# Kernel tuning notes

Hardware: AMD Instinct MI355X
Metric: run time of the kernel (lower is better)

The kernel has to match this reference:

```python
import jax, jax.numpy as jnp
import numpy as np

N, E = 50000, 600000
D_IN, D_H, D_OUT, D_E = 128, 128, 128, 32


def setup_inputs() -> dict:
    key = jax.random.key(0)
    ks = jax.random.split(key, 20)
    s = 0.05
    inp = {
        "x": jax.random.normal(ks[0], (N, D_IN), dtype=jnp.float32),
        "edge_index": jax.random.randint(ks[1], (2, E), 0, N, dtype=jnp.int64),
        "edge_attr": jax.random.normal(ks[2], (E, D_E), dtype=jnp.float32),
        # layer 0 (GINEConv MLP + edge lin: edge_dim -> in_channels)
        "w1_0": jax.random.normal(ks[3], (D_IN, D_H), dtype=jnp.float32) * s,
        "b1_0": jnp.zeros((D_H,), jnp.float32),
        "w2_0": jax.random.normal(ks[4], (D_H, D_H), dtype=jnp.float32) * s,
        "b2_0": jnp.zeros((D_H,), jnp.float32),
        "we_0": jax.random.normal(ks[5], (D_E, D_IN), dtype=jnp.float32) * s,
        "be_0": jnp.zeros((D_IN,), jnp.float32),
        # layer 1 (edge lin: edge_dim -> hidden_channels)
        "w1_1": jax.random.normal(ks[6], (D_H, D_H), dtype=jnp.float32) * s,
        "b1_1": jnp.zeros((D_H,), jnp.float32),
        "w2_1": jax.random.normal(ks[7], (D_H, D_H), dtype=jnp.float32) * s,
        "b2_1": jnp.zeros((D_H,), jnp.float32),
        "we_1": jax.random.normal(ks[8], (D_E, D_H), dtype=jnp.float32) * s,
        "be_1": jnp.zeros((D_H,), jnp.float32),
        # output head
        "fc1_w": jax.random.normal(ks[9], (D_H, D_H), dtype=jnp.float32) * s,
        "fc1_b": jnp.zeros((D_H,), jnp.float32),
        "fc2_w": jax.random.normal(ks[10], (D_H, D_OUT), dtype=jnp.float32) * s,
        "fc2_b": jnp.zeros((D_OUT,), jnp.float32),
    }
    return inp


def _gine_layer(x, src, dst, edge_attr, we, be, w1, b1, w2, b2):
    # GINEConv (eps=0): out = MLP(x + sum_j ReLU(x_j + edge_lin(e_ij)))
    e_emb = edge_attr @ we + be                       # [E, d]
    msg = jax.nn.relu(x[src] + e_emb)                 # gather + message
    agg = jax.ops.segment_sum(msg, dst, num_segments=x.shape[0])  # scatter-add
    h = agg + x                                       # (1 + eps) * x, eps = 0
    return jnp.maximum(h @ w1 + b1, 0.0) @ w2 + b2    # 2-layer MLP


def reference(x, edge_index, edge_attr,
              w1_0, b1_0, w2_0, b2_0, we_0, be_0,
              w1_1, b1_1, w2_1, b2_1, we_1, be_1,
              fc1_w, fc1_b, fc2_w, fc2_b):
    src, dst = edge_index[0], edge_index[1]
    h = _gine_layer(x, src, dst, edge_attr, we_0, be_0, w1_0, b1_0, w2_0, b2_0)
    h = jax.nn.relu(h)  # activation (dropout=0 -> identity)
    h = _gine_layer(h, src, dst, edge_attr, we_1, be_1, w1_1, b1_1, w2_1, b2_1)
    h = jax.nn.relu(h)
    h = jax.nn.relu(h @ fc1_w + fc1_b)
    return h @ fc2_w + fc2_b
```

## Files before the change

### kernel.cpp

```cpp
#include <hip/hip_runtime.h>
#include <stdint.h>


#define ND 128
#define ED 32

typedef __attribute__((ext_vector_type(8))) short short8;
typedef __attribute__((ext_vector_type(4))) float f32x4;

__device__ inline unsigned short bf16_hi(float f) {
    union { float f; unsigned u; } v;
    v.f = f;
    return (unsigned short)(v.u >> 16);
}
__device__ inline float bf16_f(unsigned short h) {
    union { unsigned u; float f; } v;
    v.u = ((unsigned)h) << 16;
    return v.f;
}

__global__ __launch_bounds__(256) void zero_kernel(int* __restrict__ p, int n) {
    int i = blockIdx.x * blockDim.x + threadIdx.x;
    if (i < n) p[i] = 0;
}

__global__ __launch_bounds__(256) void hist_kernel(const int* __restrict__ ei,
                                                   int* __restrict__ counts, int E) {
    int i = blockIdx.x * blockDim.x + threadIdx.x;
    if (i < E) atomicAdd(&counts[ei[E + i]], 1);
}

__global__ __launch_bounds__(256) void bsum_kernel(const int* __restrict__ counts,
                                                   int* __restrict__ bsum, int N) {
    __shared__ int s[256];
    int t = threadIdx.x;
    int i = blockIdx.x * 256 + t;
    s[t] = (i < N) ? counts[i] : 0;
    __syncthreads();
#pragma unroll
    for (int off = 128; off > 0; off >>= 1) {
        if (t < off) s[t] += s[t + off];
        __syncthreads();
    }
    if (t == 0) bsum[blockIdx.x] = s[0];
}

__global__ __launch_bounds__(256) void scan_bsums(const int* __restrict__ bsum,
                                                  int* __restrict__ bofs,
                                                  int* __restrict__ row_start_N, int NB) {
    __shared__ int s[256];
    int t = threadIdx.x;
    int chunk = (NB + 255) >> 8;
    int lo = min(t * chunk, NB);
    int hi = min(lo + chunk, NB);
    int sum = 0;
    for (int i = lo; i < hi; ++i) sum += bsum[i];
    s[t] = sum;
    __syncthreads();
    for (int off = 1; off < 256; off <<= 1) {
        int v = (t >= off) ? s[t - off] : 0;
        __syncthreads();
        s[t] += v;
        __syncthreads();
    }
    int pre = (t == 0) ? 0 : s[t - 1];
    for (int i = lo; i < hi; ++i) {
        bofs[i] = pre;
        pre += bsum[i];
    }
    if (t == 255) *row_start_N = s[255];
}

__global__ __launch_bounds__(256) void expand_kernel(const int* __restrict__ counts,
                                                     const int* __restrict__ bofs,
                                                     int* __restrict__ row_start,
                                                     int* __restrict__ woff, int N) {
    __shared__ int s[256];
    int t = threadIdx.x;
    int i = blockIdx.x * 256 + t;
    int c = (i < N) ? counts[i] : 0;
    s[t] = c;
    __syncthreads();
    for (int off = 1; off < 256; off <<= 1) {
        int v = (t >= off) ? s[t - off] : 0;
        __syncthreads();
        s[t] += v;
        __syncthreads();
    }
    if (i < N) {
        int pre = bofs[blockIdx.x] + s[t] - c;
        row_start[i] = pre;
        woff[i] = pre;
    }
}

__global__ __launch_bounds__(256) void scatter_kernel(const int* __restrict__ ei,
                                                      int* __restrict__ woff,
                                                      int4* __restrict__ pack, int E) {
    int i = blockIdx.x * blockDim.x + threadIdx.x;
    if (i < E) {
        int d = ei[E + i];
        int p = atomicAdd(&woff[d], 1);
        pack[p] = make_int4(ei[i], i, d, 0);
    }
}

__global__ __launch_bounds__(256) void wprep_kernel(
    const float* __restrict__ w0, const float* __restrict__ w1,
    const float* __restrict__ w2, const float* __restrict__ w3,
    const float* __restrict__ w4, const float* __restrict__ w5,
    unsigned short* __restrict__ hi, unsigned short* __restrict__ lo) {
    int t = blockIdx.x * blockDim.x + threadIdx.x;
    const float* W;
    switch (blockIdx.y) {
        case 0: W = w0; break;
        case 1: W = w1; break;
        case 2: W = w2; break;
        case 3: W = w3; break;
        case 4: W = w4; break;
        default: W = w5; break;
    }
    unsigned short* dh = hi + (size_t)blockIdx.y * 16384;
    unsigned short* dl = lo + (size_t)blockIdx.y * 16384;
    int c = t >> 6, l = t & 63;
    int nt = c >> 2, ks = c & 3;
    int n = nt * 16 + (l & 15);
    int kb = ks * 32 + ((l >> 4) << 3);
#pragma unroll
    for (int j = 0; j < 8; ++j) {
        float f = W[(size_t)(kb + j) * ND + n];
        unsigned short h = bf16_hi(f);
        dh[((size_t)c * 64 + l) * 8 + j] = h;
        dl[((size_t)c * 64 + l) * 8 + j] = bf16_hi(f - bf16_f(h));
    }
}

__global__ __launch_bounds__(256) void wprep_we(const float* __restrict__ w0,
                                                const float* __restrict__ w1,
                                                unsigned short* __restrict__ hi) {
    int t = threadIdx.x;
    int c = (blockIdx.x << 2) + (t >> 6);
    int l = t & 63;
    const float* W = blockIdx.y ? w1 : w0;
    unsigned short* dh = hi + (size_t)blockIdx.y * 4096;
    int n = c * 16 + (l & 15);
    int kb = (l >> 4) << 3;
#pragma unroll
    for (int j = 0; j < 8; ++j)
        dh[((size_t)c * 64 + l) * 8 + j] = bf16_hi(W[(size_t)(kb + j) * ND + n]);
}

__global__ __launch_bounds__(256, 4) void agg_mfma(
    const float* __restrict__ xin, const float* __restrict__ edge_attr,
    const unsigned short* __restrict__ bfh, const float* __restrict__ be,
    const int* __restrict__ row_start, const int4* __restrict__ pack,
    float* __restrict__ hout, int N, int NW) {
    int lane = threadIdx.x & 63;
    int gw = (blockIdx.x * blockDim.x + threadIdx.x) >> 6;
    int m = lane & 15;
    int quad = lane >> 4;

    short8 bh[8];
#pragma unroll
    for (int nt = 0; nt < 8; ++nt)
        bh[nt] = *(const short8*)(bfh + ((size_t)nt * 64 + lane) * 8);
    float ber[8];
#pragma unroll
    for (int nt = 0; nt < 8; ++nt) ber[nt] = be[nt * 16 + m];

    for (int v = gw; v < N; v += NW) {
        int beg = row_start[v];
        int end = row_start[v + 1];
        float part[8];
#pragma unroll
        for (int nt = 0; nt < 8; ++nt) part[nt] = 0.f;

        for (int base = beg; base < end; base += 16) {
            int rem = end - base;
            int mm = m < rem ? m : rem - 1;
            int4 pk = pack[base + mm];
            int s[4];
#pragma unroll
            for (int r = 0; r < 4; ++r) s[r] = __shfl(pk.x, quad * 4 + r, 64);

            const float4* ar = (const float4*)(edge_attr + (size_t)pk.y * ED + quad * 8);
            float4 a0 = ar[0], a1 = ar[1];
            float xv[4][8];
#pragma unroll
            for (int r = 0; r < 4; ++r) {
                const float* xr = xin + (size_t)s[r] * ND + m;
#pragma unroll
                for (int nt = 0; nt < 8; ++nt) xv[r][nt] = xr[nt * 16];
            }

            float af[8] = {a0.x, a0.y, a0.z, a0.w, a1.x, a1.y, a1.z, a1.w};
            short8 ah, al;
#pragma unroll
            for (int j = 0; j < 8; ++j) {
                unsigned short h = bf16_hi(af[j]);
                ah[j] = (short)h;
                al[j] = (short)bf16_hi(af[j] - bf16_f(h));
            }

#pragma unroll
            for (int nt = 0; nt < 8; ++nt) {
                f32x4 a = {0.f, 0.f, 0.f, 0.f};
                a = __builtin_amdgcn_mfma_f32_16x16x32_bf16(ah, bh[nt], a, 0, 0, 0);
                a = __builtin_amdgcn_mfma_f32_16x16x32_bf16(al, bh[nt], a, 0, 0, 0);
#pragma unroll
                for (int r = 0; r < 4; ++r) {
                    float vm = (quad * 4 + r) < rem ? 1.f : 0.f;
                    float msg = xv[r][nt] + a[r] + ber[nt];
                    msg = msg > 0.f ? msg : 0.f;
                    part[nt] = fmaf(msg, vm, part[nt]);
                }
            }
        }
#pragma unroll
        for (int nt = 0; nt < 8; ++nt) {
            float p = part[nt];
            p += __shfl_xor(p, 16, 64);
            p += __shfl_xor(p, 32, 64);
            part[nt] = p;
        }
        float o0 = quad == 0 ? part[0] : quad == 1 ? part[2] : quad == 2 ? part[4] : part[6];
        float o1 = quad == 0 ? part[1] : quad == 1 ? part[3] : quad == 2 ? part[5] : part[7];
        int col0 = quad * 32 + m;
        int col1 = col0 + 16;
        hout[(size_t)v * ND + col0] = xin[(size_t)v * ND + col0] + o0;
        hout[(size_t)v * ND + col1] = xin[(size_t)v * ND + col1] + o1;
    }
}

#define LP 132
__global__ __launch_bounds__(256, 4) void mlp2_mfma(
    const float* __restrict__ A,
    const unsigned short* __restrict__ w1h, const unsigned short* __restrict__ w1l,
    const float* __restrict__ b1,
    const unsigned short* __restrict__ w2h, const unsigned short* __restrict__ w2l,
    const float* __restrict__ b2,
    float* __restrict__ C, int N, int relu2) {
    __shared__ float tile[4][16 * LP];
    int lane = threadIdx.x & 63;
    int wave = threadIdx.x >> 6;
    int gw = blockIdx.x * 4 + wave;
    int m0 = gw * 16;
    if (m0 >= N) return;
    int m = lane & 15;
    int quad = lane >> 4;
    float* T = tile[wave];

    int row = m0 + m;
    bool rok = row < N;
    short8 ah[4], al[4];
#pragma unroll
    for (int ks = 0; ks < 4; ++ks) {
        float f[8];
        if (rok) {
            const float4* p = (const float4*)(A + (size_t)row * ND + ks * 32 + quad * 8);
            float4 a0 = p[0], a1 = p[1];
            f[0] = a0.x; f[1] = a0.y; f[2] = a0.z; f[3] = a0.w;
            f[4] = a1.x; f[5] = a1.y; f[6] = a1.z; f[7] = a1.w;
        } else {
#pragma unroll
            for (int j = 0; j < 8; ++j) f[j] = 0.f;
        }
#pragma unroll
        for (int j = 0; j < 8; ++j) {
            unsigned short hh = bf16_hi(f[j]);
            ah[ks][j] = (short)hh;
            al[ks][j] = (short)bf16_hi(f[j] - bf16_f(hh));
        }
    }

#pragma unroll
    for (int nt = 0; nt < 8; ++nt) {
        f32x4 acc = {0.f, 0.f, 0.f, 0.f};
#pragma unroll
        for (int ks = 0; ks < 4; ++ks) {
            size_t off = ((size_t)(nt * 4 + ks) * 64 + lane) * 8;
            short8 bh = *(const short8*)(w1h + off);
            short8 bl = *(const short8*)(w1l + off);
            acc = __builtin_amdgcn_mfma_f32_16x16x32_bf16(ah[ks], bh, acc, 0, 0, 0);
            acc = __builtin_amdgcn_mfma_f32_16x16x32_bf16(al[ks], bh, acc, 0, 0, 0);
            acc = __builtin_amdgcn_mfma_f32_16x16x32_bf16(ah[ks], bl, acc, 0, 0, 0);
        }
        float bv = b1[nt * 16 + m];
#pragma unroll
        for (int r = 0; r < 4; ++r) {
            float o = acc[r] + bv;
            o = o > 0.f ? o : 0.f;
            T[(quad * 4 + r) * LP + nt * 16 + m] = o;
        }
    }

    short8 ch[4], cl[4];
#pragma unroll
    for (int ks = 0; ks < 4; ++ks) {
        const float4* p = (const float4*)(T + m * LP + ks * 32 + quad * 8);
        float4 a0 = p[0], a1 = p[1];
        float f[8] = {a0.x, a0.y, a0.z, a0.w, a1.x, a1.y, a1.z, a1.w};
#pragma unroll
        for (int j = 0; j < 8; ++j) {
            unsigned short hh = bf16_hi(f[j]);
            ch[ks][j] = (short)hh;
            cl[ks][j] = (short)bf16_hi(f[j] - bf16_f(hh));
        }
    }

#pragma unroll
    for (int nt = 0; nt < 8; ++nt) {
        f32x4 acc = {0.f, 0.f, 0.f, 0.f};
#pragma unroll
        for (int ks = 0; ks < 4; ++ks) {
            size_t off = ((size_t)(nt * 4 + ks) * 64 + lane) * 8;
            short8 bh = *(const short8*)(w2h + off);
            short8 bl = *(const short8*)(w2l + off);
            acc = __builtin_amdgcn_mfma_f32_16x16x32_bf16(ch[ks], bh, acc, 0, 0, 0);
            acc = __builtin_amdgcn_mfma_f32_16x16x32_bf16(cl[ks], bh, acc, 0, 0, 0);
            acc = __builtin_amdgcn_mfma_f32_16x16x32_bf16(ch[ks], bl, acc, 0, 0, 0);
        }
        float bv = b2[nt * 16 + m];
#pragma unroll
        for (int r = 0; r < 4; ++r) {
            int rr = m0 + quad * 4 + r;
            if (rr < N) {
                float o = acc[r] + bv;
                if (relu2) o = o > 0.f ? o : 0.f;
                C[(size_t)rr * ND + nt * 16 + m] = o;
            }
        }
    }
}

extern "C" void kernel_launch(void* const* d_in, const int* in_sizes, int n_in,
                              void* d_out, int out_size, void* d_ws, size_t ws_size,
                              hipStream_t stream) {
    const float* x = (const float*)d_in[0];
    const int* ei = (const int*)d_in[1];
    const float* ea = (const float*)d_in[2];
    const float* w1_0 = (const float*)d_in[3];
    const float* b1_0 = (const float*)d_in[4];
    const float* w2_0 = (const float*)d_in[5];
    const float* b2_0 = (const float*)d_in[6];
    const float* we_0 = (const float*)d_in[7];
    const float* be_0 = (const float*)d_in[8];
    const float* w1_1 = (const float*)d_in[9];
    const float* b1_1 = (const float*)d_in[10];
    const float* w2_1 = (const float*)d_in[11];
    const float* b2_1 = (const float*)d_in[12];
    const float* we_1 = (const float*)d_in[13];
    const float* be_1 = (const float*)d_in[14];
    const float* fc1_w = (const float*)d_in[15];
    const float* fc1_b = (const float*)d_in[16];
    const float* fc2_w = (const float*)d_in[17];
    const float* fc2_b = (const float*)d_in[18];

    int N = in_sizes[0] / ND;
    int E = in_sizes[2] / ED;
    int NB = (N + 255) / 256;

    float* bufA = (float*)d_ws;
    int* counts = (int*)(bufA + (size_t)N * ND);
    int* row_start = counts + N;
    int* woff = row_start + (N + 1);
    int* bsum = woff + N;
    int* bofs = bsum + NB;
    int4* pack = (int4*)((((uintptr_t)(bofs + NB)) + 15) & ~(uintptr_t)15);
    unsigned short* wfh = (unsigned short*)(pack + E);
    unsigned short* wfl = wfh + 6 * 16384;
    unsigned short* weh = wfl + 6 * 16384;
    float* out = (float*)d_out;

    zero_kernel<<<(N + 255) / 256, 256, 0, stream>>>(counts, N);
    hist_kernel<<<(E + 255) / 256, 256, 0, stream>>>(ei, counts, E);
    bsum_kernel<<<NB, 256, 0, stream>>>(counts, bsum, N);
    scan_bsums<<<1, 256, 0, stream>>>(bsum, bofs, row_start + N, NB);
    expand_kernel<<<NB, 256, 0, stream>>>(counts, bofs, row_start, woff, N);
    scatter_kernel<<<(E + 255) / 256, 256, 0, stream>>>(ei, woff, pack, E);
    wprep_kernel<<<dim3(8, 6), 256, 0, stream>>>(w1_0, w2_0, w1_1, w2_1, fc1_w, fc2_w,
                                                 wfh, wfl);
    wprep_we<<<dim3(2, 2), 256, 0, stream>>>(we_0, we_1, weh);

    const int NW = 4096;
    int gg = ((N + 15) / 16 + 3) / 4;

    agg_mfma<<<NW / 4, 256, 0, stream>>>(x, ea, weh, be_0, row_start, pack, out, N, NW);
    mlp2_mfma<<<gg, 256, 0, stream>>>(out, wfh + 0 * 16384, wfl + 0 * 16384, b1_0,
                                      wfh + 1 * 16384, wfl + 1 * 16384, b2_0, bufA, N, 1);

    agg_mfma<<<NW / 4, 256, 0, stream>>>(bufA, ea, weh + 4096, be_1, row_start, pack, out,
                                         N, NW);
    mlp2_mfma<<<gg, 256, 0, stream>>>(out, wfh + 2 * 16384, wfl + 2 * 16384, b1_1,
                                      wfh + 3 * 16384, wfl + 3 * 16384, b2_1, bufA, N, 1);

    mlp2_mfma<<<gg, 256, 0, stream>>>(bufA, wfh + 4 * 16384, wfl + 4 * 16384, fc1_b,
                                      wfh + 5 * 16384, wfl + 5 * 16384, fc2_b, out, N, 0);
}
```

Measured before the change: 470.8 us.

## Shrink edge pack to int2, double agg occupancy, split MLP columns across wave pairs

The CSR edge pack drops from int4 to int2 (src, edge id), which halves the bytes written by the scatter and read by aggregation. The aggregation kernel's launch bound asks for 8 blocks per CU and the persistent wave count doubles to 8192. The 2-layer MLP kernel now uses 512-thread blocks where two waves share each 16-row tile, each computing half of the output columns, with a block barrier between the layers. The goal is more parallelism and latency hiding, at the cost of register pressure in aggregation and redundant A-tile loads in the MLP.

```diff
diff --git a/kernel.cpp b/kernel.cpp
--- a/kernel.cpp
+++ b/kernel.cpp
@@ -96,12 +96,12 @@
 
 __global__ __launch_bounds__(256) void scatter_kernel(const int* __restrict__ ei,
                                                       int* __restrict__ woff,
-                                                      int4* __restrict__ pack, int E) {
+                                                      int2* __restrict__ pack, int E) {
     int i = blockIdx.x * blockDim.x + threadIdx.x;
     if (i < E) {
         int d = ei[E + i];
         int p = atomicAdd(&woff[d], 1);
-        pack[p] = make_int4(ei[i], i, d, 0);
+        pack[p] = make_int2(ei[i], i);
     }
 }
 
@@ -150,10 +150,10 @@
         dh[((size_t)c * 64 + l) * 8 + j] = bf16_hi(W[(size_t)(kb + j) * ND + n]);
 }
 
-__global__ __launch_bounds__(256, 4) void agg_mfma(
+__global__ __launch_bounds__(256, 8) void agg_mfma(
     const float* __restrict__ xin, const float* __restrict__ edge_attr,
     const unsigned short* __restrict__ bfh, const float* __restrict__ be,
-    const int* __restrict__ row_start, const int4* __restrict__ pack,
+    const int* __restrict__ row_start, const int2* __restrict__ pack,
     float* __restrict__ hout, int N, int NW) {
     int lane = threadIdx.x & 63;
     int gw = (blockIdx.x * blockDim.x + threadIdx.x) >> 6;
@@ -178,7 +178,7 @@
         for (int base = beg; base < end; base += 16) {
             int rem = end - base;
             int mm = m < rem ? m : rem - 1;
-            int4 pk = pack[base + mm];
+            int2 pk = pack[base + mm];
             int s[4];
 #pragma unroll
             for (int r = 0; r < 4; ++r) s[r] = __shfl(pk.x, quad * 4 + r, 64);
@@ -233,7 +233,7 @@
 }
 
 #define LP 132
-__global__ __launch_bounds__(256, 4) void mlp2_mfma(
+__global__ __launch_bounds__(512, 4) void mlp2_mfma(
     const float* __restrict__ A,
     const unsigned short* __restrict__ w1h, const unsigned short* __restrict__ w1l,
     const float* __restrict__ b1,
@@ -241,14 +241,15 @@
     const float* __restrict__ b2,
     float* __restrict__ C, int N, int relu2) {
     __shared__ float tile[4][16 * LP];
-    int lane = threadIdx.x & 63;
-    int wave = threadIdx.x >> 6;
-    int gw = blockIdx.x * 4 + wave;
-    int m0 = gw * 16;
-    if (m0 >= N) return;
+    int t = threadIdx.x;
+    int lane = t & 63;
+    int wave = t >> 6;
+    int pair = wave >> 1;
+    int half = wave & 1;
+    int m0 = (blockIdx.x * 4 + pair) * 16;
     int m = lane & 15;
     int quad = lane >> 4;
-    float* T = tile[wave];
+    float* T = tile[pair];
 
     int row = m0 + m;
     bool rok = row < N;
@@ -274,7 +275,8 @@
     }
 
 #pragma unroll
-    for (int nt = 0; nt < 8; ++nt) {
+    for (int ntl = 0; ntl < 4; ++ntl) {
+        int nt = half * 4 + ntl;
         f32x4 acc = {0.f, 0.f, 0.f, 0.f};
 #pragma unroll
         for (int ks = 0; ks < 4; ++ks) {
@@ -294,6 +296,8 @@
         }
     }
 
+    __syncthreads();
+
     short8 ch[4], cl[4];
 #pragma unroll
     for (int ks = 0; ks < 4; ++ks) {
@@ -309,7 +313,8 @@
     }
 
 #pragma unroll
-    for (int nt = 0; nt < 8; ++nt) {
+    for (int ntl = 0; ntl < 4; ++ntl) {
+        int nt = half * 4 + ntl;
         f32x4 acc = {0.f, 0.f, 0.f, 0.f};
 #pragma unroll
         for (int ks = 0; ks < 4; ++ks) {
@@ -366,7 +371,7 @@
     int* woff = row_start + (N + 1);
     int* bsum = woff + N;
     int* bofs = bsum + NB;
-    int4* pack = (int4*)((((uintptr_t)(bofs + NB)) + 15) & ~(uintptr_t)15);
+    int2* pack = (int2*)((((uintptr_t)(bofs + NB)) + 15) & ~(uintptr_t)15);
     unsigned short* wfh = (unsigned short*)(pack + E);
     unsigned short* wfl = wfh + 6 * 16384;
     unsigned short* weh = wfl + 6 * 16384;
@@ -382,18 +387,18 @@
                                                  wfh, wfl);
     wprep_we<<<dim3(2, 2), 256, 0, stream>>>(we_0, we_1, weh);
 
-    const int NW = 4096;
-    int gg = ((N + 15) / 16 + 3) / 4;
+    const int NW = 8192;
+    int gg = (N + 63) / 64;
 
     agg_mfma<<<NW / 4, 256, 0, stream>>>(x, ea, weh, be_0, row_start, pack, out, N, NW);
-    mlp2_mfma<<<gg, 256, 0, stream>>>(out, wfh + 0 * 16384, wfl + 0 * 16384, b1_0,
+    mlp2_mfma<<<gg, 512, 0, stream>>>(out, wfh + 0 * 16384, wfl + 0 * 16384, b1_0,
                                       wfh + 1 * 16384, wfl + 1 * 16384, b2_0, bufA, N, 1);
 
     agg_mfma<<<NW / 4, 256, 0, stream>>>(bufA, ea, weh + 4096, be_1, row_start, pack, out,
                                          N, NW);
-    mlp2_mfma<<<gg, 256, 0, stream>>>(out, wfh + 2 * 16384, wfl + 2 * 16384, b1_1,
+    mlp2_mfma<<<gg, 512, 0, stream>>>(out, wfh + 2 * 16384, wfl + 2 * 16384, b1_1,
                                       wfh + 3 * 16384, wfl + 3 * 16384, b2_1, bufA, N, 1);
 
-    mlp2_mfma<<<gg, 256, 0, stream>>>(bufA, wfh + 4 * 16384, wfl + 4 * 16384, fc1_b,
+    mlp2_mfma<<<gg, 512, 0, stream>>>(bufA, wfh + 4 * 16384, wfl + 4 * 16384, fc1_b,
                                       wfh + 5 * 16384, wfl + 5 * 16384, fc2_b, out, N, 0);
 }
```

After: 1.078 ms. +129.0%, slower.
